# Performance work log

Hardware: AMD Instinct MI355X
Metric: run time of the kernel (lower is better)

## Reference

```python
import jax, jax.numpy as jnp
import numpy as np

DIM = 512
HEADS = 8
DIM_HEAD = 64
INNER = HEADS * DIM_HEAD  # 512
SCALE = DIM_HEAD ** -0.5


def setup_inputs() -> dict:
    key = jax.random.key(0)
    k1, k2, k3, k4 = jax.random.split(key, 4)
    x = jax.random.normal(k1, (4, 2048, DIM), dtype=jnp.float32)
    # Dense(inner_dim*3, use_bias=False): weight [dim, 3*inner]
    w_qkv = jax.random.normal(k2, (DIM, 3 * INNER), dtype=jnp.float32) * (DIM ** -0.5)
    # to_out Dense(dim): weight [inner, dim] + bias [dim]
    w_out = jax.random.normal(k3, (INNER, DIM), dtype=jnp.float32) * (INNER ** -0.5)
    b_out = jax.random.normal(k4, (DIM,), dtype=jnp.float32) * 0.01
    return {"x": x, "w_qkv": w_qkv, "w_out": w_out, "b_out": b_out}


def reference(x, w_qkv, w_out, b_out):
    b, n, _ = x.shape
    qkv = x @ w_qkv                                  # [b, n, 3*inner]
    q, k, v = jnp.split(qkv, 3, axis=-1)             # each [b, n, inner]
    def to_heads(t):
        return t.reshape(b, n, HEADS, DIM_HEAD).transpose(0, 2, 1, 3)  # [b, h, n, d]
    q, k, v = map(to_heads, (q, k, v))
    dots = jnp.einsum('bhid,bhjd->bhij', q, k) * SCALE
    attn = jax.nn.softmax(dots, axis=-1)
    out = jnp.einsum('bhij,bhjd->bhid', attn, v)     # [b, h, n, d]
    out = out.transpose(0, 2, 1, 3).reshape(b, n, INNER)
    return out @ w_out + b_out                       # [b, n, dim]
```

## Files before the change

kernel.cpp:

```cpp
#include <hip/hip_runtime.h>
#include <stdint.h>

#define DIM    512
#define HEADS  8
#define DHEAD  64
#define SEQ    2048
#define BATCH  4
#define BH     (BATCH*HEADS)
#define MROWS  (BATCH*SEQ)
#define NQKV   (3*DIM)
#define QSCALE 0.18033688011112042f

typedef __bf16 bf16x8 __attribute__((ext_vector_type(8)));
typedef float  f32x4  __attribute__((ext_vector_type(4)));

typedef unsigned short u16;

#if __has_builtin(__builtin_amdgcn_exp2f)
#define EXP2(x) __builtin_amdgcn_exp2f(x)
#else
#define EXP2(x) exp2f(x)
#endif

__device__ __forceinline__ u16 f2bf(float f) {
    union { float f; uint32_t u; } v; v.f = f;
    uint32_t u = v.u;
    uint32_t r = (u + 0x7FFFu + ((u >> 16) & 1u)) >> 16;
    return (u16)r;
}
__device__ __forceinline__ float bf2f(u16 h) {
    union { uint32_t u; float f; } v; v.u = ((uint32_t)h) << 16;
    return v.f;
}
__device__ __forceinline__ uint32_t pk2bf(float a, float b) {
    union { float f; uint32_t u; } ua, ub; ua.f = a; ub.f = b;
#if __has_builtin(__builtin_amdgcn_perm)
    return __builtin_amdgcn_perm(ub.u + 0x8000u, ua.u + 0x8000u, 0x07060302u);
#else
    return ((ua.u + 0x8000u) >> 16) | ((ub.u + 0x8000u) & 0xFFFF0000u);
#endif
}

__device__ __forceinline__ void async16(const void* g, u16* l) {
    __builtin_amdgcn_global_load_lds(
        (const __attribute__((address_space(1))) void*)g,
        (__attribute__((address_space(3))) void*)l, 16, 0, 0);
}

#define XBLKS (MROWS * DIM / 4 / 256)
#define WQT   ((DIM / 64) * (NQKV / 64))
#define WOT   ((DIM / 64) * (DIM / 64))
__global__ void prep(const void* __restrict__ x, const void* __restrict__ wq,
                     const void* __restrict__ wo, u16* __restrict__ xb,
                     u16* __restrict__ wtq, u16* __restrict__ wto,
                     int* __restrict__ flag) {
    __shared__ int cnt;
    __shared__ __align__(16) u16 tile[64][72];
    int tid = threadIdx.x;
    if (tid == 0) cnt = 0;
    __syncthreads();
    {
        u16 v = ((const u16*)x)[tid * 2];
        int e = (v >> 7) & 0xFF;
        atomicAdd(&cnt, (v == 0) || (e >= 100 && e <= 140));
    }
    __syncthreads();
    int isbf = (cnt >= 192);
    int b = blockIdx.x;
    if (b == 0 && tid == 0) *flag = isbf;

    if (b < XBLKS) {
        int i = b * 256 + tid;
        if (isbf) {
            ((uint2*)xb)[i] = ((const uint2*)x)[i];
        } else {
            float4 v = ((const float4*)x)[i];
            ushort4 o;
            o.x = f2bf(v.x); o.y = f2bf(v.y); o.z = f2bf(v.z); o.w = f2bf(v.w);
            ((ushort4*)xb)[i] = o;
        }
        return;
    }
    const void* W; u16* Wt; int N, tb;
    if (b < XBLKS + WQT) { W = wq; Wt = wtq; N = NQKV; tb = b - XBLKS; }
    else                 { W = wo; Wt = wto; N = DIM;  tb = b - XBLKS - WQT; }
    int tn = N / 64;
    int k0 = (tb / tn) * 64, n0 = (tb - (tb / tn) * tn) * 64;

#pragma unroll 4
    for (int it = 0; it < 16; ++it) {
        int idx = it * 256 + tid;
        int r = idx >> 6, c = idx & 63;
        u16 v = isbf ? ((const u16*)W)[(size_t)(k0 + r) * N + n0 + c]
                     : f2bf(((const float*)W)[(size_t)(k0 + r) * N + n0 + c]);
        tile[c][r] = v;
    }
    __syncthreads();
    {
        int n = tid >> 2, ks = (tid & 3) * 16;
        uint4 v0 = *(const uint4*)&tile[n][ks];
        uint4 v1 = *(const uint4*)&tile[n][ks + 8];
        *(uint4*)&Wt[(size_t)(n0 + n) * DIM + k0 + ks] = v0;
        *(uint4*)&Wt[(size_t)(n0 + n) * DIM + k0 + ks + 8] = v1;
    }
}

template<int KDIM, int TM, int TN>
__device__ __forceinline__ void gemm_lds_db(
        const u16* __restrict__ A, const u16* __restrict__ Bt,
        int m0, int n0, int tid, u16* As, u16* Bs,
        f32x4 (&acc)[TM / 32][TN / 32]) {
    int lane = tid & 63, ln = lane & 15, quad = lane >> 4, w = tid >> 6;
    int wm = (w >> 1) * (TM / 2), wn = (w & 1) * (TN / 2);

    auto stage = [&](int buf, int k0) {
#pragma unroll
        for (int ii = 0; ii < TM / 64; ++ii) {
            int r0 = (ii * 4 + w) * 16;
            int row = r0 + (lane >> 2);
            int seg = (lane & 3) ^ (row & 3);
            async16(A + (size_t)(m0 + row) * KDIM + k0 + seg * 8,
                    As + buf * TM * 32 + r0 * 32);
        }
#pragma unroll
        for (int ii = 0; ii < TN / 64; ++ii) {
            int r0 = (ii * 4 + w) * 16;
            int row = r0 + (lane >> 2);
            int seg = (lane & 3) ^ (row & 3);
            async16(Bt + (size_t)(n0 + row) * KDIM + k0 + seg * 8,
                    Bs + buf * TN * 32 + r0 * 32);
        }
    };

    stage(0, 0);
#pragma unroll 1
    for (int kk = 0; kk < KDIM / 32; ++kk) {
        __syncthreads();
        if (kk + 1 < KDIM / 32) stage((kk + 1) & 1, (kk + 1) * 32);
        const u16* Ac = As + (kk & 1) * TM * 32;
        const u16* Bc = Bs + (kk & 1) * TN * 32;
        bf16x8 a[TM / 32], b[TN / 32];
        int rseg = (quad ^ (ln & 3)) * 8;
#pragma unroll
        for (int i = 0; i < TM / 32; ++i)
            a[i] = *(const bf16x8*)(Ac + (wm + i * 16 + ln) * 32 + rseg);
#pragma unroll
        for (int j = 0; j < TN / 32; ++j)
            b[j] = *(const bf16x8*)(Bc + (wn + j * 16 + ln) * 32 + rseg);
#pragma unroll
        for (int i = 0; i < TM / 32; ++i)
#pragma unroll
            for (int j = 0; j < TN / 32; ++j)
                acc[i][j] = __builtin_amdgcn_mfma_f32_16x16x32_bf16(
                    a[i], b[j], acc[i][j], 0, 0, 0);
    }
}

__global__ __launch_bounds__(256, 3) void qkv_gemm(
        const u16* __restrict__ X, const u16* __restrict__ Wt,
        u16* __restrict__ Qt, u16* __restrict__ Kb, u16* __restrict__ Vt) {
    __shared__ __align__(16) u16 As[2 * 128 * 32];
    __shared__ __align__(16) u16 Bs[2 * 128 * 32];

    int tid  = threadIdx.x;
    int lane = tid & 63, ln = lane & 15, quad = lane >> 4, wid = tid >> 6;
    int m0 = blockIdx.x * 128, n0 = blockIdx.y * 128;
    int wm = (wid >> 1) * 64, wn = (wid & 1) * 64;

    f32x4 acc[4][4];
#pragma unroll
    for (int i = 0; i < 4; ++i)
#pragma unroll
        for (int j = 0; j < 4; ++j) acc[i][j] = 0.f;

    gemm_lds_db<DIM, 128, 128>(X, Wt, m0, n0, tid, As, Bs, acc);

#pragma unroll
    for (int j = 0; j < 4; ++j) {
        int col   = n0 + wn + j * 16 + ln;
        int which = col >> 9;
        int hd    = col & 511;
        int h     = hd >> 6, d = hd & 63;
#pragma unroll
        for (int i = 0; i < 4; ++i) {
            int rbase = m0 + wm + i * 16 + quad * 4;
            int b = rbase >> 11, n = rbase & 2047;
            int bh = b * HEADS + h;
            if (which == 1) {
#pragma unroll
                for (int r = 0; r < 4; ++r)
                    Kb[((size_t)bh * SEQ + n + r) * DHEAD + d] = f2bf(acc[i][j][r]);
            } else {
                float s = (which == 0) ? QSCALE : 1.0f;
                uint2 pv;
                pv.x = pk2bf(acc[i][j][0] * s, acc[i][j][1] * s);
                pv.y = pk2bf(acc[i][j][2] * s, acc[i][j][3] * s);
                u16* dst = (which == 0) ? Qt : Vt;
                *(uint2*)&dst[((size_t)bh * DHEAD + d) * SEQ + n] = pv;
            }
        }
    }
}

__global__ __launch_bounds__(256, 2) void flash_attn(
        const u16* __restrict__ Qt, const u16* __restrict__ Kb,
        const u16* __restrict__ Vt, u16* __restrict__ Ob) {
    __shared__ __align__(16) u16 Kc[2][64 * 64];
    __shared__ __align__(16) u16 Vc[2][64 * 64];
    __shared__ __align__(16) u16 Pl[4][32 * 64];

    int tid  = threadIdx.x;
    int lane = tid & 63, ln = lane & 15, quad = lane >> 4, wid = tid >> 6;
    int bh = blockIdx.x;
    int q0 = blockIdx.y * 128 + wid * 32;

    const u16* Qh = Qt + (size_t)bh * SEQ * DHEAD;
    const u16* Kh = Kb + (size_t)bh * SEQ * DHEAD;
    const u16* Vh = Vt + (size_t)bh * DHEAD * SEQ;

    int srow = lane >> 3;
    int gseg = (lane & 7) ^ srow;

    auto stageKV = [&](int buf, int kc) {
#pragma unroll
        for (int ii = 0; ii < 2; ++ii) {
            int slab = wid + ii * 4;
            const u16* gk = Kh + (size_t)(kc + slab * 8 + srow) * DHEAD + gseg * 8;
            async16(gk, &Kc[buf][slab * 8 * 64]);
            const u16* gv = Vh + (size_t)(slab * 8 + srow) * SEQ + kc + gseg * 8;
            async16(gv, &Vc[buf][slab * 8 * 64]);
        }
    };

    bf16x8 qf[2][2];
#pragma unroll
    for (int qt = 0; qt < 2; ++qt)
#pragma unroll
        for (int s = 0; s < 2; ++s) {
            union { u16 a[8]; bf16x8 v; } u;
#pragma unroll
            for (int jj = 0; jj < 8; ++jj)
                u.a[jj] = Qh[(size_t)(s * 32 + quad * 8 + jj) * SEQ + q0 + qt * 16 + ln];
            qf[qt][s] = u.v;
        }

    f32x4 o[2][4];
#pragma unroll
    for (int qt = 0; qt < 2; ++qt)
#pragma unroll
        for (int t = 0; t < 4; ++t) o[qt][t] = 0.f;
    float lsum[2] = {0.f, 0.f};

    stageKV(0, 0);
    __syncthreads();

#pragma unroll 1
    for (int kc = 0; kc < SEQ; kc += 64) {
        int cur = (kc >> 6) & 1;
        if (kc + 64 < SEQ) stageKV(cur ^ 1, kc + 64);

        bf16x8 kf[4][2], vf[4][2];
#pragma unroll
        for (int kt = 0; kt < 4; ++kt) {
            int row = kt * 16 + ln;
#pragma unroll
            for (int s = 0; s < 2; ++s) {
                int seg = (s * 4 + quad) ^ (ln & 7);
                kf[kt][s] = *(const bf16x8*)&Kc[cur][row * 64 + seg * 8];
                vf[kt][s] = *(const bf16x8*)&Vc[cur][row * 64 + seg * 8];
            }
        }

        f32x4 st[4][2];
#pragma unroll
        for (int kt = 0; kt < 4; ++kt)
#pragma unroll
            for (int qt = 0; qt < 2; ++qt) st[kt][qt] = 0.f;
#pragma unroll
        for (int kt = 0; kt < 4; ++kt)
#pragma unroll
            for (int qt = 0; qt < 2; ++qt)
#pragma unroll
                for (int s = 0; s < 2; ++s)
                    st[kt][qt] = __builtin_amdgcn_mfma_f32_16x16x32_bf16(
                        kf[kt][s], qf[qt][s], st[kt][qt], 0, 0, 0);

#pragma unroll
        for (int qt = 0; qt < 2; ++qt)
#pragma unroll
            for (int kt = 0; kt < 4; ++kt) {
                float p0 = EXP2(st[kt][qt][0]);
                float p1 = EXP2(st[kt][qt][1]);
                float p2 = EXP2(st[kt][qt][2]);
                float p3 = EXP2(st[kt][qt][3]);
                lsum[qt] += (p0 + p1) + (p2 + p3);
                uint2 d;
                d.x = pk2bf(p0, p1);
                d.y = pk2bf(p2, p3);
                int seg = (kt * 2 + (quad >> 1)) ^ (ln & 7);
                *(uint2*)&Pl[wid][(qt * 16 + ln) * 64 + seg * 8 + (quad & 1) * 4] = d;
            }

        bf16x8 pf[2][2];
#pragma unroll
        for (int qt = 0; qt < 2; ++qt)
#pragma unroll
            for (int s = 0; s < 2; ++s) {
                int seg = (s * 4 + quad) ^ (ln & 7);
                pf[qt][s] = *(const bf16x8*)&Pl[wid][(qt * 16 + ln) * 64 + seg * 8];
            }

#pragma unroll
        for (int t = 0; t < 4; ++t)
#pragma unroll
            for (int s = 0; s < 2; ++s)
#pragma unroll
                for (int qt = 0; qt < 2; ++qt)
                    o[qt][t] = __builtin_amdgcn_mfma_f32_16x16x32_bf16(
                        pf[qt][s], vf[t][s], o[qt][t], 0, 0, 0);

        __syncthreads();
    }

#pragma unroll
    for (int qt = 0; qt < 2; ++qt) {
        float s = lsum[qt];
        s += __shfl_xor(s, 16);
        s += __shfl_xor(s, 32);
        lsum[qt] = 1.0f / s;
    }

    int b = bh >> 3, h = bh & 7;
#pragma unroll
    for (int qt = 0; qt < 2; ++qt) {
#pragma unroll
        for (int t = 0; t < 4; ++t) {
            int d = t * 16 + ln;
#pragma unroll
            for (int r = 0; r < 4; ++r) {
                int qrow = quad * 4 + r;
                float inv = __shfl(lsum[qt], qrow);
                int n = q0 + qt * 16 + qrow;
                Ob[((size_t)(b * SEQ + n)) * DIM + h * DHEAD + d] =
                    f2bf(o[qt][t][r] * inv);
            }
        }
    }
}

__global__ __launch_bounds__(256, 3) void out_gemm(
        const u16* __restrict__ A, const u16* __restrict__ Wt,
        const void* __restrict__ bias, void* __restrict__ out,
        const int* __restrict__ flag) {
    __shared__ __align__(16) u16 As[2 * 64 * 32];
    __shared__ __align__(16) u16 Bs[2 * 128 * 32];

    int tid  = threadIdx.x;
    int lane = tid & 63, ln = lane & 15, quad = lane >> 4, wid = tid >> 6;
    int m0 = blockIdx.x * 64, n0 = blockIdx.y * 128;
    int wm = (wid >> 1) * 32, wn = (wid & 1) * 64;
    int isbf = *flag;

    f32x4 acc[2][4];
#pragma unroll
    for (int i = 0; i < 2; ++i)
#pragma unroll
        for (int j = 0; j < 4; ++j) acc[i][j] = 0.f;

    gemm_lds_db<DIM, 64, 128>(A, Wt, m0, n0, tid, As, Bs, acc);

#pragma unroll
    for (int j = 0; j < 4; ++j) {
        int col = n0 + wn + j * 16 + ln;
        float bv = isbf ? bf2f(((const u16*)bias)[col])
                        : ((const float*)bias)[col];
#pragma unroll
        for (int i = 0; i < 2; ++i) {
            int rbase = m0 + wm + i * 16 + quad * 4;
#pragma unroll
            for (int r = 0; r < 4; ++r) {
                int row = rbase + r;
                size_t off = (size_t)row * DIM + col;
                float val = acc[i][j][r] + bv;
                if (isbf) ((u16*)out)[off] = f2bf(val);
                else      ((float*)out)[off] = val;
            }
        }
    }
}

extern "C" void kernel_launch(void* const* d_in, const int* in_sizes, int n_in,
                              void* d_out, int out_size, void* d_ws, size_t ws_size,
                              hipStream_t stream) {
    const void* x     = d_in[0];
    const void* w_qkv = d_in[1];
    const void* w_out = d_in[2];
    const void* b_out = d_in[3];

    int* flag   = (int*)d_ws;
    u16* x_bf   = (u16*)((char*)d_ws + 16);
    u16* wt_qkv = x_bf + (size_t)MROWS * DIM;
    u16* wt_out = wt_qkv + (size_t)NQKV * DIM;
    u16* Qt     = wt_out + (size_t)DIM * DIM;
    u16* Kb     = Qt + (size_t)BH * SEQ * DHEAD;
    u16* Vt     = Kb + (size_t)BH * SEQ * DHEAD;
    u16* attn   = x_bf;

    prep<<<XBLKS + WQT + WOT, 256, 0, stream>>>(
        x, w_qkv, w_out, x_bf, wt_qkv, wt_out, flag);
    qkv_gemm<<<dim3(MROWS / 128, NQKV / 128), 256, 0, stream>>>(x_bf, wt_qkv, Qt, Kb, Vt);
    flash_attn<<<dim3(BH, SEQ / 128), 256, 0, stream>>>(Qt, Kb, Vt, attn);
    out_gemm<<<dim3(MROWS / 64, DIM / 128), 256, 0, stream>>>(attn, wt_out, b_out, d_out, flag);
}
```

Measured before the change: 176.7 us.

## Rewrite flash attention with 32x32x16 MFMA and register-only P via permlane32 swap

The attention kernel moves from 16x16x32 to 32x32x16 bf16 MFMA tiles and doubles the queries per wave to 64. The exponentiated scores are repacked in registers with v_permlane32_swap as the A operand of the PV matmul, which removes the per-wave LDS round trip for P. The row sums are computed by an extra MFMA against a vector of ones instead of scalar adds and shuffles. The cost is higher register pressure (launch bounds drop to 1 block/SM), half as many blocks, and a different XOR swizzle for K/V staging.

```diff
diff --git a/kernel.cpp b/kernel.cpp
--- a/kernel.cpp
+++ b/kernel.cpp
@@ -13,6 +13,7 @@
 
 typedef __bf16 bf16x8 __attribute__((ext_vector_type(8)));
 typedef float  f32x4  __attribute__((ext_vector_type(4)));
+typedef float  f32x16 __attribute__((ext_vector_type(16)));
 
 typedef unsigned short u16;
 
@@ -40,6 +41,8 @@
     return ((ua.u + 0x8000u) >> 16) | ((ub.u + 0x8000u) & 0xFFFF0000u);
 #endif
 }
+
+#define P32SWAP(x, y) asm("v_permlane32_swap_b32 %0, %1" : "+v"(x), "+v"(y))
 
 __device__ __forceinline__ void async16(const void* g, u16* l) {
     __builtin_amdgcn_global_load_lds(
@@ -202,149 +205,137 @@
     }
 }
 
-__global__ __launch_bounds__(256, 2) void flash_attn(
+__global__ __launch_bounds__(256, 1) void flash_attn(
         const u16* __restrict__ Qt, const u16* __restrict__ Kb,
         const u16* __restrict__ Vt, u16* __restrict__ Ob) {
     __shared__ __align__(16) u16 Kc[2][64 * 64];
     __shared__ __align__(16) u16 Vc[2][64 * 64];
-    __shared__ __align__(16) u16 Pl[4][32 * 64];
 
     int tid  = threadIdx.x;
-    int lane = tid & 63, ln = lane & 15, quad = lane >> 4, wid = tid >> 6;
+    int lane = tid & 63, c = lane & 31, hi = lane >> 5, wid = tid >> 6;
     int bh = blockIdx.x;
-    int q0 = blockIdx.y * 128 + wid * 32;
+    int q0 = blockIdx.y * 256 + wid * 64;
 
     const u16* Qh = Qt + (size_t)bh * SEQ * DHEAD;
     const u16* Kh = Kb + (size_t)bh * SEQ * DHEAD;
     const u16* Vh = Vt + (size_t)bh * DHEAD * SEQ;
 
     int srow = lane >> 3;
-    int gseg = (lane & 7) ^ srow;
-
     auto stageKV = [&](int buf, int kc) {
 #pragma unroll
         for (int ii = 0; ii < 2; ++ii) {
             int slab = wid + ii * 4;
-            const u16* gk = Kh + (size_t)(kc + slab * 8 + srow) * DHEAD + gseg * 8;
+            int g = (lane & 7) ^ srow ^ (slab & 3);
+            const u16* gk = Kh + (size_t)(kc + slab * 8 + srow) * DHEAD + g * 8;
             async16(gk, &Kc[buf][slab * 8 * 64]);
-            const u16* gv = Vh + (size_t)(slab * 8 + srow) * SEQ + kc + gseg * 8;
+            const u16* gv = Vh + (size_t)(slab * 8 + srow) * SEQ + kc + g * 8;
             async16(gv, &Vc[buf][slab * 8 * 64]);
         }
     };
 
-    bf16x8 qf[2][2];
-#pragma unroll
-    for (int qt = 0; qt < 2; ++qt)
-#pragma unroll
-        for (int s = 0; s < 2; ++s) {
+    bf16x8 qf[2][4];
+#pragma unroll
+    for (int qg = 0; qg < 2; ++qg)
+#pragma unroll
+        for (int ds = 0; ds < 4; ++ds) {
             union { u16 a[8]; bf16x8 v; } u;
 #pragma unroll
-            for (int jj = 0; jj < 8; ++jj)
-                u.a[jj] = Qh[(size_t)(s * 32 + quad * 8 + jj) * SEQ + q0 + qt * 16 + ln];
-            qf[qt][s] = u.v;
-        }
-
-    f32x4 o[2][4];
-#pragma unroll
-    for (int qt = 0; qt < 2; ++qt)
-#pragma unroll
-        for (int t = 0; t < 4; ++t) o[qt][t] = 0.f;
-    float lsum[2] = {0.f, 0.f};
+            for (int j = 0; j < 8; ++j)
+                u.a[j] = Qh[(size_t)(ds * 16 + hi * 8 + j) * SEQ + q0 + qg * 32 + c];
+            qf[qg][ds] = u.v;
+        }
+
+    bf16x8 onesf;
+    { union { uint32_t d[4]; bf16x8 v; } u;
+      u.d[0] = u.d[1] = u.d[2] = u.d[3] = 0x3F803F80u; onesf = u.v; }
+
+    f32x16 o[2][2];
+    f32x16 lacc[2];
+#pragma unroll
+    for (int qg = 0; qg < 2; ++qg) {
+        lacc[qg] = 0.f;
+#pragma unroll
+        for (int dt = 0; dt < 2; ++dt) o[qg][dt] = 0.f;
+    }
 
     stageKV(0, 0);
     __syncthreads();
+
+    int fl = (c & 7) ^ ((c >> 3) & 3);
 
 #pragma unroll 1
     for (int kc = 0; kc < SEQ; kc += 64) {
         int cur = (kc >> 6) & 1;
         if (kc + 64 < SEQ) stageKV(cur ^ 1, kc + 64);
 
-        bf16x8 kf[4][2], vf[4][2];
-#pragma unroll
-        for (int kt = 0; kt < 4; ++kt) {
-            int row = kt * 16 + ln;
-#pragma unroll
-            for (int s = 0; s < 2; ++s) {
-                int seg = (s * 4 + quad) ^ (ln & 7);
-                kf[kt][s] = *(const bf16x8*)&Kc[cur][row * 64 + seg * 8];
-                vf[kt][s] = *(const bf16x8*)&Vc[cur][row * 64 + seg * 8];
-            }
-        }
-
-        f32x4 st[4][2];
-#pragma unroll
-        for (int kt = 0; kt < 4; ++kt)
-#pragma unroll
-            for (int qt = 0; qt < 2; ++qt) st[kt][qt] = 0.f;
-#pragma unroll
-        for (int kt = 0; kt < 4; ++kt)
-#pragma unroll
-            for (int qt = 0; qt < 2; ++qt)
-#pragma unroll
-                for (int s = 0; s < 2; ++s)
-                    st[kt][qt] = __builtin_amdgcn_mfma_f32_16x16x32_bf16(
-                        kf[kt][s], qf[qt][s], st[kt][qt], 0, 0, 0);
-
-#pragma unroll
-        for (int qt = 0; qt < 2; ++qt)
-#pragma unroll
-            for (int kt = 0; kt < 4; ++kt) {
-                float p0 = EXP2(st[kt][qt][0]);
-                float p1 = EXP2(st[kt][qt][1]);
-                float p2 = EXP2(st[kt][qt][2]);
-                float p3 = EXP2(st[kt][qt][3]);
-                lsum[qt] += (p0 + p1) + (p2 + p3);
-                uint2 d;
-                d.x = pk2bf(p0, p1);
-                d.y = pk2bf(p2, p3);
-                int seg = (kt * 2 + (quad >> 1)) ^ (ln & 7);
-                *(uint2*)&Pl[wid][(qt * 16 + ln) * 64 + seg * 8 + (quad & 1) * 4] = d;
-            }
-
-        bf16x8 pf[2][2];
-#pragma unroll
-        for (int qt = 0; qt < 2; ++qt)
-#pragma unroll
-            for (int s = 0; s < 2; ++s) {
-                int seg = (s * 4 + quad) ^ (ln & 7);
-                pf[qt][s] = *(const bf16x8*)&Pl[wid][(qt * 16 + ln) * 64 + seg * 8];
-            }
-
-#pragma unroll
-        for (int t = 0; t < 4; ++t)
-#pragma unroll
-            for (int s = 0; s < 2; ++s)
-#pragma unroll
-                for (int qt = 0; qt < 2; ++qt)
-                    o[qt][t] = __builtin_amdgcn_mfma_f32_16x16x32_bf16(
-                        pf[qt][s], vf[t][s], o[qt][t], 0, 0, 0);
-
+#pragma unroll
+        for (int kt = 0; kt < 2; ++kt) {
+            bf16x8 kf[4];
+#pragma unroll
+            for (int ds = 0; ds < 4; ++ds) {
+                int slot = (ds * 2 + hi) ^ fl;
+                kf[ds] = *(const bf16x8*)&Kc[cur][(kt * 32 + c) * 64 + slot * 8];
+            }
+
+            bf16x8 pa[2][2];
+#pragma unroll
+            for (int qg = 0; qg < 2; ++qg) {
+                f32x16 s;
+                s = 0.f;
+#pragma unroll
+                for (int ds = 0; ds < 4; ++ds)
+                    s = __builtin_amdgcn_mfma_f32_32x32x16_bf16(
+                        kf[ds], qf[qg][ds], s, 0, 0, 0);
+                float p[16];
+#pragma unroll
+                for (int r = 0; r < 16; ++r) p[r] = EXP2(s[r]);
+                uint32_t X[8];
+#pragma unroll
+                for (int i = 0; i < 8; ++i) X[i] = pk2bf(p[2 * i], p[2 * i + 1]);
+                P32SWAP(X[0], X[2]); P32SWAP(X[1], X[3]);
+                P32SWAP(X[4], X[6]); P32SWAP(X[5], X[7]);
+                union { uint32_t d[4]; bf16x8 v; } u0, u1;
+                u0.d[0] = X[0]; u0.d[1] = X[1]; u0.d[2] = X[2]; u0.d[3] = X[3];
+                u1.d[0] = X[4]; u1.d[1] = X[5]; u1.d[2] = X[6]; u1.d[3] = X[7];
+                pa[qg][0] = u0.v; pa[qg][1] = u1.v;
+            }
+
+#pragma unroll
+            for (int tl = 0; tl < 2; ++tl) {
+#pragma unroll
+                for (int dt = 0; dt < 2; ++dt) {
+                    int slot = ((kt * 2 + tl) * 2 + hi) ^ fl;
+                    bf16x8 vf = *(const bf16x8*)&Vc[cur][(dt * 32 + c) * 64 + slot * 8];
+#pragma unroll
+                    for (int qg = 0; qg < 2; ++qg)
+                        o[qg][dt] = __builtin_amdgcn_mfma_f32_32x32x16_bf16(
+                            pa[qg][tl], vf, o[qg][dt], 0, 0, 0);
+                }
+#pragma unroll
+                for (int qg = 0; qg < 2; ++qg)
+                    lacc[qg] = __builtin_amdgcn_mfma_f32_32x32x16_bf16(
+                        pa[qg][tl], onesf, lacc[qg], 0, 0, 0);
+            }
+        }
         __syncthreads();
     }
 
-#pragma unroll
-    for (int qt = 0; qt < 2; ++qt) {
-        float s = lsum[qt];
-        s += __shfl_xor(s, 16);
-        s += __shfl_xor(s, 32);
-        lsum[qt] = 1.0f / s;
-    }
-
-    int b = bh >> 3, h = bh & 7;
-#pragma unroll
-    for (int qt = 0; qt < 2; ++qt) {
-#pragma unroll
-        for (int t = 0; t < 4; ++t) {
-            int d = t * 16 + ln;
-#pragma unroll
-            for (int r = 0; r < 4; ++r) {
-                int qrow = quad * 4 + r;
-                float inv = __shfl(lsum[qt], qrow);
-                int n = q0 + qt * 16 + qrow;
-                Ob[((size_t)(b * SEQ + n)) * DIM + h * DHEAD + d] =
-                    f2bf(o[qt][t][r] * inv);
-            }
-        }
+    int b = bh >> 3, hh = bh & 7;
+#pragma unroll
+    for (int qg = 0; qg < 2; ++qg) {
+        f32x16 linv;
+#pragma unroll
+        for (int r = 0; r < 16; ++r) linv[r] = 1.0f / lacc[qg][r];
+#pragma unroll
+        for (int dt = 0; dt < 2; ++dt)
+#pragma unroll
+            for (int r = 0; r < 16; ++r) {
+                int ql = (r & 3) + 8 * (r >> 2) + 4 * hi;
+                int n  = q0 + qg * 32 + ql;
+                int d  = dt * 32 + c;
+                Ob[((size_t)(b * SEQ + n)) * DIM + hh * DHEAD + d] =
+                    f2bf(o[qg][dt][r] * linv[r]);
+            }
     }
 }
 
@@ -409,6 +400,6 @@
     prep<<<XBLKS + WQT + WOT, 256, 0, stream>>>(
         x, w_qkv, w_out, x_bf, wt_qkv, wt_out, flag);
     qkv_gemm<<<dim3(MROWS / 128, NQKV / 128), 256, 0, stream>>>(x_bf, wt_qkv, Qt, Kb, Vt);
-    flash_attn<<<dim3(BH, SEQ / 128), 256, 0, stream>>>(Qt, Kb, Vt, attn);
+    flash_attn<<<dim3(BH, SEQ / 256), 256, 0, stream>>>(Qt, Kb, Vt, attn);
     out_gemm<<<dim3(MROWS / 64, DIM / 128), 256, 0, stream>>>(attn, wt_out, b_out, d_out, flag);
 }
```

Result: slower. 191.8 us (+8.6%).
